# Performance work log

Measured on AMD Instinct MI355X. Metric: run time of the kernel, lower is better.

## Reference

```python
import jax, jax.numpy as jnp
import numpy as np

N = 100000
E = 1_600_000
DIN = 24
DH = 64
DOUT = 12
NEG_SLOPE = 0.01  # torch F.leaky_relu default


def setup_inputs() -> dict:
    key = jax.random.key(0)
    ks = jax.random.split(key, 18)
    inp = {}
    inp["feats"] = jax.random.normal(ks[0], (N, DIN), dtype=jnp.float32)
    inp["e_w"] = jax.random.uniform(ks[1], (E, 1), dtype=jnp.float32)
    inp["snorm_n"] = jnp.ones((N, 1), dtype=jnp.float32)
    inp["snorm_e"] = jnp.ones((E, 1), dtype=jnp.float32)
    inp["src"] = jax.random.randint(ks[2], (E,), 0, N, dtype=jnp.int32)
    inp["dst"] = jax.random.randint(ks[3], (E,), 0, N, dtype=jnp.int32)
    s = 0.05
    inp["emb_h_W"] = jax.random.normal(ks[4], (DH, DIN), dtype=jnp.float32) * s
    inp["emb_h_b"] = jnp.zeros((DH,), dtype=jnp.float32)
    inp["emb_e_W"] = jax.random.normal(ks[5], (DH, 1), dtype=jnp.float32) * s
    inp["emb_e_b"] = jnp.zeros((DH,), dtype=jnp.float32)
    inp["W_self1"] = jax.random.normal(ks[6], (DH, DH), dtype=jnp.float32) * s
    inp["W_func1"] = jax.random.normal(ks[7], (DH, DH), dtype=jnp.float32) * s
    inp["attn1"] = jax.random.normal(ks[8], (3 * DH,), dtype=jnp.float32) * s
    inp["W_self2"] = jax.random.normal(ks[9], (DH, DH), dtype=jnp.float32) * s
    inp["W_func2"] = jax.random.normal(ks[10], (DH, DH), dtype=jnp.float32) * s
    inp["attn2"] = jax.random.normal(ks[11], (3 * DH,), dtype=jnp.float32) * s
    inp["lin1_W"] = jax.random.normal(ks[12], (DOUT, DH), dtype=jnp.float32) * s
    inp["lin1_b"] = jnp.zeros((DOUT,), dtype=jnp.float32)
    return inp


def _gat_layer(h, w_edge, src, dst, W_self, W_func, attn):
    # h: [N, d], w_edge: [E, d] edge embedding, attn: [3d]
    h_s = h @ W_self.T                       # linear_self(h)
    z = h @ W_func.T                         # linear_func(h)
    d = z.shape[-1]
    a_src, a_dst, a_w = attn[:d], attn[d:2 * d], attn[2 * d:]
    # attention score: W_a . [z_src, z_dst, w]  (decomposed to avoid [E,3d] concat)
    s_node_src = z @ a_src                   # [N]
    s_node_dst = z @ a_dst                   # [N]
    e = s_node_src[src] + s_node_dst[dst] + w_edge @ a_w  # [E]
    e = jax.nn.leaky_relu(e, NEG_SLOPE)
    # segment softmax over incoming edges per destination node
    m = jax.ops.segment_max(e, dst, num_segments=h.shape[0])
    ex = jnp.exp(e - m[dst])
    denom = jax.ops.segment_sum(ex, dst, num_segments=h.shape[0])
    alpha = ex / denom[dst]                  # [E]
    msg = alpha[:, None] * z[src]            # [E, d]
    agg = jax.ops.segment_sum(msg, dst, num_segments=h.shape[0])  # [N, d]
    # DGL: nodes with no incoming edges keep their old 'h' (not h_s + agg)
    in_deg = jax.ops.segment_sum(jnp.ones_like(e), dst, num_segments=h.shape[0])
    h_mid = jnp.where((in_deg > 0)[:, None], h_s + agg, h)
    return h + jax.nn.relu(h_mid)            # relu then residual


def reference(feats, e_w, snorm_n, snorm_e, src, dst,
              emb_h_W, emb_h_b, emb_e_W, emb_e_b,
              W_self1, W_func1, attn1, W_self2, W_func2, attn2,
              lin1_W, lin1_b):
    feats = feats.reshape(feats.shape[0], -1)
    h = feats @ emb_h_W.T + emb_h_b          # [N, DH]
    e = e_w @ emb_e_W.T + emb_e_b            # [E, DH]
    h = _gat_layer(h, e, src, dst, W_self1, W_func1, attn1)
    h = _gat_layer(h, e, src, dst, W_self2, W_func2, attn2)
    y = h @ lin1_W.T + lin1_b                # [N, DOUT]
    return y
```

## Files before the change

kernel.cpp:

```cpp
#include <hip/hip_runtime.h>
#include <hip/hip_fp16.h>

#define N_NODES 100000
#define N_EDGES 1600000
#define DIN 24
#define DH 64
#define DOUT 12
#define NEG_SLOPE 0.01f
#define NG 64
#define EPG (N_EDGES / NG)
#define NS 4
#define SLICE_N 32768
#define NTOT (NG * N_NODES)
#define SCAN_BLK 4096
#define LDSW 72

#define NB_HIST (NS * NG)
#define NB_SUMDEG ((N_NODES + 255) / 256)
#define NB_SCAN1N ((N_NODES + SCAN_BLK - 1) / SCAN_BLK)
#define NB_SCAT ((N_EDGES / 4 + 255) / 256)
#define NB_NODE ((N_NODES + 63) / 64)
#define NB_NODE_T ((NB_NODE + 1) / 2)
#define NB_NME ((NB_NODE + 7) / 8)
#define NB_AGG ((N_NODES + 7) / 8)

#define SM_WEMB 18432
#define SM_BIAS 23552
#define SM_HBUF 23808
#define SM_SIZE 60672

typedef _Float16 half8_t __attribute__((ext_vector_type(8)));
typedef float floatx4 __attribute__((ext_vector_type(4)));

__device__ __forceinline__ void dev_consts(const float* emb_e_W, const float* emb_e_b,
                                           const float* attn1, const float* attn2,
                                           float* consts) {
    int lane = threadIdx.x;
    if (lane >= 64) return;
    float w = emb_e_W[lane], b = emb_e_b[lane];
    float a1 = attn1[2 * DH + lane], a2 = attn2[2 * DH + lane];
    float c11 = w * a1, c01 = b * a1, c12 = w * a2, c02 = b * a2;
    for (int off = 32; off; off >>= 1) {
        c11 += __shfl_down(c11, off);
        c01 += __shfl_down(c01, off);
        c12 += __shfl_down(c12, off);
        c02 += __shfl_down(c02, off);
    }
    if (lane == 0) {
        consts[0] = c11; consts[1] = c01; consts[2] = c12; consts[3] = c02;
    }
}

__device__ __forceinline__ void dev_hist(int bid, char* smem, const int* dst,
                                         unsigned char* deg, unsigned char* rank) {
    unsigned* cnt = (unsigned*)smem;
    int s = bid % NS, c = bid / NS;
    for (int i = threadIdx.x; i < SLICE_N / 4; i += 1024) cnt[i] = 0;
    __syncthreads();
    int nbase = s * SLICE_N;
    int start = c * EPG, end = start + EPG;
    for (int i = start + threadIdx.x; i < end; i += 1024) {
        int local = dst[i] - nbase;
        if ((unsigned)local < SLICE_N) {
            unsigned sh = (unsigned)(local & 3) * 8u;
            unsigned old = atomicAdd(&cnt[local >> 2], 1u << sh);
            rank[i] = (unsigned char)((old >> sh) & 255u);
        }
    }
    __syncthreads();
    int nmax = N_NODES - nbase;
    if (nmax > SLICE_N) nmax = SLICE_N;
    unsigned* dw = (unsigned*)(deg + (size_t)c * N_NODES + nbase);
    for (int l = threadIdx.x; l < (nmax >> 2); l += 1024) dw[l] = cnt[l];
}

__device__ __forceinline__ void dev_scan1(int bid, const int* in, int* out,
                                          int* part, int n) {
    __shared__ int lds[256];
    int t = threadIdx.x;
    int base = bid * SCAN_BLK + t * 16;
    int v[16];
    int s = 0;
#pragma unroll
    for (int i = 0; i < 16; ++i) {
        int idx = base + i;
        v[i] = (idx < n) ? in[idx] : 0;
        s += v[i];
    }
    lds[t] = s;
    __syncthreads();
    for (int off = 1; off < 256; off <<= 1) {
        int y = (t >= off) ? lds[t - off] : 0;
        __syncthreads();
        lds[t] += y;
        __syncthreads();
    }
    int run = lds[t] - s;
#pragma unroll
    for (int i = 0; i < 16; ++i) {
        int idx = base + i;
        if (idx < n) out[idx] = run;
        run += v[i];
    }
    if (t == 255) part[bid] = lds[255];
}

__device__ __forceinline__ void dev_sumdeg(int bid, const unsigned char* degB,
                                           int* degN, unsigned char* chunkOff) {
    int n = bid * 256 + threadIdx.x;
    if (n >= N_NODES) return;
    int run = 0;
    for (int g = 0; g < NG; ++g) {
        size_t idx = (size_t)g * N_NODES + n;
        int v = (int)degB[idx];
        chunkOff[idx] = (unsigned char)run;
        run += v;
    }
    degN[n] = run;
}

__device__ __forceinline__ void dev_nodeME(int bid, char* smem,
                                           const float* feats, const float* embW,
                                           const float* embB,
                                           const float* Wself, const float* Wfunc,
                                           const float* attn,
                                           __half* h16, __half* zh, __half* hs16,
                                           float* s_src, float* s_dst) {
    _Float16* lds   = (_Float16*)smem;
    _Float16* wembH = (_Float16*)(smem + SM_WEMB);
    float*    biasS = (float*)(smem + SM_BIAS);
    _Float16* hbufA = (_Float16*)(smem + SM_HBUF);
    int tid = threadIdx.x;
    for (int idx = tid; idx < 2 * 64 * 64; idx += 1024) {
        int mat = idx >> 12, rem = idx & 4095;
        int o = rem >> 6, k = rem & 63;
        float v = mat ? Wfunc[rem] : Wself[rem];
        lds[(mat * 64 + o) * LDSW + k] = (_Float16)v;
    }
    for (int idx = tid; idx < 64 * 32; idx += 1024) {
        int o = idx >> 5, k = idx & 31;
        wembH[o * 40 + k] = (_Float16)((k < DIN) ? embW[o * DIN + k] : 0.f);
    }
    if (tid < 64) biasS[tid] = embB[tid];
    __syncthreads();

    int wave = tid >> 6, lane = tid & 63;
    int vb = wave >> 2, wv = wave & 3;
    int quad = lane >> 4, lm = lane & 15;
    float asv[4], adv[4];
#pragma unroll
    for (int t = 0; t < 4; ++t) {
        asv[t] = attn[t * 16 + lm];
        adv[t] = attn[DH + t * 16 + lm];
    }
    const _Float16* bS = lds;
    const _Float16* bF = lds + 64 * LDSW;
    _Float16* hb = hbufA + wave * (16 * 72);

    for (int tb = bid * 4 + vb; tb < NB_NODE; tb += NB_NME * 4) {
        int n0 = (tb * 4 + wv) * 16;
        if (n0 >= N_NODES) continue;

        half8_t afE;
#pragma unroll
        for (int j = 0; j < 8; ++j) afE[j] = (_Float16)0.f;
        if (quad < 3) {
            const float* f = feats + (size_t)(n0 + lm) * DIN + quad * 8;
            float4 q0 = *(const float4*)(f);
            float4 q1 = *(const float4*)(f + 4);
            afE[0] = (_Float16)q0.x; afE[1] = (_Float16)q0.y;
            afE[2] = (_Float16)q0.z; afE[3] = (_Float16)q0.w;
            afE[4] = (_Float16)q1.x; afE[5] = (_Float16)q1.y;
            afE[6] = (_Float16)q1.z; afE[7] = (_Float16)q1.w;
        }
        floatx4 accE[4];
#pragma unroll
        for (int t = 0; t < 4; ++t) accE[t] = (floatx4)0.f;
#pragma unroll
        for (int t = 0; t < 4; ++t) {
            int o = t * 16 + lm;
            half8_t bE = *(const half8_t*)(wembH + o * 40 + quad * 8);
            accE[t] = __builtin_amdgcn_mfma_f32_16x16x32_f16(afE, bE, accE[t], 0, 0, 0);
        }
#pragma unroll
        for (int t = 0; t < 4; ++t) {
            float bv = biasS[t * 16 + lm];
#pragma unroll
            for (int r = 0; r < 4; ++r) {
                float hv = accE[t][r] + bv;
                int node = n0 + quad * 4 + r;
                h16[(size_t)node * DH + t * 16 + lm] = __float2half(hv);
                hb[(quad * 4 + r) * 72 + t * 16 + lm] = (_Float16)hv;
            }
        }
        half8_t afrag[2];
#pragma unroll
        for (int ks = 0; ks < 2; ++ks)
            afrag[ks] = *(const half8_t*)(hb + lm * 72 + ks * 32 + quad * 8);

        floatx4 accS[4], accF[4];
#pragma unroll
        for (int t = 0; t < 4; ++t) { accS[t] = (floatx4)0.f; accF[t] = (floatx4)0.f; }
#pragma unroll
        for (int t = 0; t < 4; ++t) {
            int o = t * 16 + lm;
#pragma unroll
            for (int ks = 0; ks < 2; ++ks) {
                int hoff = o * LDSW + ks * 32 + quad * 8;
                half8_t b1 = *(const half8_t*)(bS + hoff);
                half8_t b2 = *(const half8_t*)(bF + hoff);
                accS[t] = __builtin_amdgcn_mfma_f32_16x16x32_f16(afrag[ks], b1, accS[t], 0, 0, 0);
                accF[t] = __builtin_amdgcn_mfma_f32_16x16x32_f16(afrag[ks], b2, accF[t], 0, 0, 0);
            }
        }

        float ps[4] = {0.f, 0.f, 0.f, 0.f}, pd[4] = {0.f, 0.f, 0.f, 0.f};
#pragma unroll
        for (int t = 0; t < 4; ++t) {
#pragma unroll
            for (int r = 0; r < 4; ++r) {
                int node = n0 + quad * 4 + r;
                float zv = accF[t][r];
                zh[(size_t)node * DH + t * 16 + lm] = __float2half(zv);
                hs16[(size_t)node * DH + t * 16 + lm] = __float2half(accS[t][r]);
                ps[r] += zv * asv[t];
                pd[r] += zv * adv[t];
            }
        }
#pragma unroll
        for (int r = 0; r < 4; ++r) {
            float p1 = ps[r], p2 = pd[r];
            for (int off = 8; off; off >>= 1) {
                p1 += __shfl_xor(p1, off);
                p2 += __shfl_xor(p2, off);
            }
            if (lm == 0) {
                s_src[n0 + quad * 4 + r] = p1;
                s_dst[n0 + quad * 4 + r] = p2;
            }
        }
    }
}

__device__ __forceinline__ void dev_nodeM(int bid, int stride, const __half* h16,
                                          const float* Wself, const float* Wfunc,
                                          const float* attn,
                                          __half* zh, __half* hs16,
                                          float* s_src, float* s_dst) {
    __shared__ _Float16 lds[2 * 64 * LDSW];
    int tid = threadIdx.x;
    for (int idx = tid; idx < 2 * 64 * 64; idx += 256) {
        int mat = idx >> 12, rem = idx & 4095;
        int o = rem >> 6, k = rem & 63;
        float v = mat ? Wfunc[rem] : Wself[rem];
        lds[(mat * 64 + o) * LDSW + k] = (_Float16)v;
    }
    __syncthreads();

    int wave = tid >> 6, lane = tid & 63;
    int quad = lane >> 4, lm = lane & 15;
    float asv[4], adv[4];
#pragma unroll
    for (int t = 0; t < 4; ++t) {
        asv[t] = attn[t * 16 + lm];
        adv[t] = attn[DH + t * 16 + lm];
    }
    const _Float16* bS = lds;
    const _Float16* bF = lds + 64 * LDSW;

    for (int tb = bid; tb < NB_NODE; tb += stride) {
        int n0 = (tb * 4 + wave) * 16;
        if (n0 >= N_NODES) continue;

        const _Float16* hrow = (const _Float16*)h16 + (size_t)(n0 + lm) * DH;
        half8_t afrag[2];
#pragma unroll
        for (int ks = 0; ks < 2; ++ks)
            afrag[ks] = *(const half8_t*)(hrow + ks * 32 + quad * 8);

        floatx4 accS[4], accF[4];
#pragma unroll
        for (int t = 0; t < 4; ++t) { accS[t] = (floatx4)0.f; accF[t] = (floatx4)0.f; }

#pragma unroll
        for (int t = 0; t < 4; ++t) {
            int o = t * 16 + lm;
#pragma unroll
            for (int ks = 0; ks < 2; ++ks) {
                int hoff = o * LDSW + ks * 32 + quad * 8;
                half8_t b1 = *(const half8_t*)(bS + hoff);
                half8_t b2 = *(const half8_t*)(bF + hoff);
                accS[t] = __builtin_amdgcn_mfma_f32_16x16x32_f16(afrag[ks], b1, accS[t], 0, 0, 0);
                accF[t] = __builtin_amdgcn_mfma_f32_16x16x32_f16(afrag[ks], b2, accF[t], 0, 0, 0);
            }
        }

        float ps[4] = {0.f, 0.f, 0.f, 0.f}, pd[4] = {0.f, 0.f, 0.f, 0.f};
#pragma unroll
        for (int t = 0; t < 4; ++t) {
#pragma unroll
            for (int r = 0; r < 4; ++r) {
                int node = n0 + quad * 4 + r;
                float zv = accF[t][r];
                zh[(size_t)node * DH + t * 16 + lm] = __float2half(zv);
                hs16[(size_t)node * DH + t * 16 + lm] = __float2half(accS[t][r]);
                ps[r] += zv * asv[t];
                pd[r] += zv * adv[t];
            }
        }
#pragma unroll
        for (int r = 0; r < 4; ++r) {
            float p1 = ps[r], p2 = pd[r];
            for (int off = 8; off; off >>= 1) {
                p1 += __shfl_xor(p1, off);
                p2 += __shfl_xor(p2, off);
            }
            if (lm == 0) {
                s_src[n0 + quad * 4 + r] = p1;
                s_dst[n0 + quad * 4 + r] = p2;
            }
        }
    }
}

__global__ void __launch_bounds__(1024, 2)
k_fuse1(const int* __restrict__ dst, unsigned char* __restrict__ deg,
        unsigned char* __restrict__ rank,
        const float* __restrict__ emb_e_W, const float* __restrict__ emb_e_b,
        const float* __restrict__ attn1, const float* __restrict__ attn2,
        float* __restrict__ consts,
        const float* __restrict__ feats, const float* __restrict__ embW,
        const float* __restrict__ embB,
        __half* __restrict__ h16, const float* __restrict__ Wself1,
        const float* __restrict__ Wfunc1,
        __half* __restrict__ zh, __half* __restrict__ hs16,
        float* __restrict__ s_src, float* __restrict__ s_dst) {
    __shared__ __align__(16) char smem[SM_SIZE];
    int bid = blockIdx.x;
    if (bid == 0) { dev_consts(emb_e_W, emb_e_b, attn1, attn2, consts); return; }
    bid -= 1;
    if (bid < NB_HIST) { dev_hist(bid, smem, dst, deg, rank); return; }
    dev_nodeME(bid - NB_HIST, smem, feats, embW, embB, Wself1, Wfunc1, attn1,
               h16, zh, hs16, s_src, s_dst);
}

__global__ void k_prep2(const unsigned char* __restrict__ degB, int* __restrict__ degN,
                        unsigned char* __restrict__ chunkOff) {
    dev_sumdeg(blockIdx.x, degB, degN, chunkOff);
}

__global__ void k_prep3(const int* __restrict__ degN, int* __restrict__ row_offN,
                        int* __restrict__ partN) {
    dev_scan1(blockIdx.x, degN, row_offN, partN, N_NODES);
}

__global__ void k_prep4(const int* __restrict__ row_offN, const int* __restrict__ partN,
                        int* __restrict__ rowStart) {
    __shared__ int pfx[32];
    int t = threadIdx.x;
    if (t < 64) {
        int v = (t < NB_SCAN1N) ? partN[t] : 0;
        int x = v;
#pragma unroll
        for (int s = 1; s < 32; s <<= 1) {
            int y = __shfl_up(x, s);
            if (t >= s) x += y;
        }
        if (t < 32) pfx[t] = x - v;
    }
    __syncthreads();
    int n = blockIdx.x * 256 + t;
    if (n < N_NODES) rowStart[n] = row_offN[n] + pfx[n >> 12];
    if (n == 0) rowStart[N_NODES] = N_EDGES;
}

__global__ void __launch_bounds__(256, 8)
k_scat(const int* __restrict__ src, const int* __restrict__ dst,
       const float* __restrict__ e_w, const unsigned char* __restrict__ rank,
       const int* __restrict__ rowStart,
       const unsigned char* __restrict__ chunkOff, unsigned* __restrict__ csr2) {
    int e4 = (blockIdx.x * 256 + threadIdx.x) * 4;
    if (e4 >= N_EDGES) return;
    int g = e4 / EPG;
    const unsigned char* co = chunkOff + (size_t)g * N_NODES;
    int4   d4 = *(const int4*)(dst + e4);
    int4   s4 = *(const int4*)(src + e4);
    float4 w4 = *(const float4*)(e_w + e4);
    unsigned r4 = *(const unsigned*)(rank + e4);
    int b0 = rowStart[d4.x] + (int)co[d4.x];
    int b1 = rowStart[d4.y] + (int)co[d4.y];
    int b2 = rowStart[d4.z] + (int)co[d4.z];
    int b3 = rowStart[d4.w] + (int)co[d4.w];
    unsigned q0 = (unsigned)(w4.x * 32768.f); if (q0 > 32767u) q0 = 32767u;
    unsigned q1 = (unsigned)(w4.y * 32768.f); if (q1 > 32767u) q1 = 32767u;
    unsigned q2 = (unsigned)(w4.z * 32768.f); if (q2 > 32767u) q2 = 32767u;
    unsigned q3 = (unsigned)(w4.w * 32768.f); if (q3 > 32767u) q3 = 32767u;
    __builtin_nontemporal_store((unsigned)s4.x | (q0 << 17), csr2 + b0 + (r4 & 255u));
    __builtin_nontemporal_store((unsigned)s4.y | (q1 << 17), csr2 + b1 + ((r4 >> 8) & 255u));
    __builtin_nontemporal_store((unsigned)s4.z | (q2 << 17), csr2 + b2 + ((r4 >> 16) & 255u));
    __builtin_nontemporal_store((unsigned)s4.w | (q3 << 17), csr2 + b3 + (r4 >> 24));
}

__global__ void __launch_bounds__(256, 4)
k_nodeL(const __half* __restrict__ h16, const float* __restrict__ Wself,
        const float* __restrict__ Wfunc, const float* __restrict__ attn,
        __half* __restrict__ zh, __half* __restrict__ hs16,
        float* __restrict__ s_src, float* __restrict__ s_dst) {
    dev_nodeM(blockIdx.x, NB_NODE_T, h16, Wself, Wfunc, attn, zh, hs16, s_src, s_dst);
}

__global__ void k_agg(const int* __restrict__ rowStart,
                      const unsigned* __restrict__ csr,
                      const float* __restrict__ s_src, const float* __restrict__ s_dstA,
                      const float* __restrict__ consts, int layer,
                      const __half* __restrict__ zh, const __half* __restrict__ hsb,
                      __half* __restrict__ h16,
                      const float* __restrict__ lin_W, const float* __restrict__ lin_b,
                      float* __restrict__ y, int final_layer) {
    int wave = threadIdx.x >> 6, lane = threadIdx.x & 63;
    int half = lane >> 5, hl = lane & 31;
    int eg = (lane >> 3) & 3, c8 = lane & 7;
    int n = blockIdx.x * 8 + wave * 2 + half;
    if (n >= N_NODES) return;
    int rs = rowStart[n];
    int deg = rowStart[n + 1] - rs;
    int degO = __shfl_xor(deg, 32);
    int degmax = deg > degO ? deg : degO;

    float c1 = consts[layer * 2 + 0];
    float c0 = consts[layer * 2 + 1];
    float sd = s_dstA[n];

    float acc[8];
#pragma unroll
    for (int k = 0; k < 8; ++k) acc[k] = 0.f;
    float ssl = 0.f;
    int lbase = lane & 32;

    for (int base = 0; base < degmax; base += 32) {
        float ex = 0.f;
        int s0 = 0;
        int idx = base + hl;
        if (idx < deg) {
            unsigned w = csr[rs + idx];
            s0 = (int)(w & 0x1FFFFu);
            float ew = (float)(w >> 17) * (1.f / 32768.f);
            float e = s_src[s0] + sd + ew * c1 + c0;
            e = (e > 0.f) ? e : NEG_SLOPE * e;
            ex = __expf(e);
        }
        ssl += ex;
        int cnt = degmax - base;
        if (cnt > 32) cnt = 32;
#pragma unroll 4
        for (int jb = 0; jb < cnt; jb += 4) {
            int srcl = lbase + jb + eg;
            int sj = __shfl(s0, srcl);
            float exj = __shfl(ex, srcl);
            unsigned boff = ((unsigned)sj << 7) | ((unsigned)c8 << 4);
            half8_t zv = *(const half8_t*)((const char*)zh + boff);
#pragma unroll
            for (int k = 0; k < 8; ++k) acc[k] += exj * (float)zv[k];
        }
    }
#pragma unroll
    for (int k = 0; k < 8; ++k) {
        acc[k] += __shfl_xor(acc[k], 8);
        acc[k] += __shfl_xor(acc[k], 16);
    }
    ssl += __shfl_xor(ssl, 16); ssl += __shfl_xor(ssl, 8);
    ssl += __shfl_xor(ssl, 4);  ssl += __shfl_xor(ssl, 2);
    ssl += __shfl_xor(ssl, 1);

    unsigned noff = ((unsigned)n << 7) | ((unsigned)c8 << 4);
    half8_t hv8 = *(const half8_t*)((const char*)h16 + noff);
    float hold[8];
#pragma unroll
    for (int k = 0; k < 8; ++k) hold[k] = (float)hv8[k];
    float hnew[8];
    if (deg == 0) {
#pragma unroll
        for (int k = 0; k < 8; ++k) hnew[k] = hold[k] + fmaxf(hold[k], 0.f);
    } else {
        float rinv = 1.f / ssl;
        half8_t hs8 = *(const half8_t*)((const char*)hsb + noff);
#pragma unroll
        for (int k = 0; k < 8; ++k)
            hnew[k] = hold[k] + fmaxf((float)hs8[k] + acc[k] * rinv, 0.f);
    }

    if (!final_layer) {
        if (eg == 0) {
            half8_t o8;
#pragma unroll
            for (int k = 0; k < 8; ++k) o8[k] = (_Float16)hnew[k];
            *(half8_t*)((char*)h16 + noff) = o8;
        }
    } else {
#pragma unroll
        for (int t = 0; t < 3; ++t) {
            int o = eg * 3 + t;
            const float* wr = lin_W + o * DH + c8 * 8;
            float p = 0.f;
#pragma unroll
            for (int k = 0; k < 8; ++k) p += hnew[k] * wr[k];
            p += __shfl_xor(p, 1); p += __shfl_xor(p, 2); p += __shfl_xor(p, 4);
            if (c8 == 0) y[n * DOUT + o] = p + lin_b[o];
        }
    }
}

extern "C" void kernel_launch(void* const* d_in, const int* in_sizes, int n_in,
                              void* d_out, int out_size, void* d_ws, size_t ws_size,
                              hipStream_t stream) {
    const float* feats   = (const float*)d_in[0];
    const float* e_w     = (const float*)d_in[1];
    const int*   src     = (const int*)d_in[4];
    const int*   dst     = (const int*)d_in[5];
    const float* emb_h_W = (const float*)d_in[6];
    const float* emb_h_b = (const float*)d_in[7];
    const float* emb_e_W = (const float*)d_in[8];
    const float* emb_e_b = (const float*)d_in[9];
    const float* Wself[2] = {(const float*)d_in[10], (const float*)d_in[13]};
    const float* Wfunc[2] = {(const float*)d_in[11], (const float*)d_in[14]};
    const float* attn[2]  = {(const float*)d_in[12], (const float*)d_in[15]};
    const float* lin1_W  = (const float*)d_in[16];
    const float* lin1_b  = (const float*)d_in[17];
    float* y = (float*)d_out;

    char* ws = (char*)d_ws;
    size_t off = 0;
    auto alloc = [&](size_t bytes) {
        void* p = ws + off;
        off += (bytes + 255) & ~(size_t)255;
        return p;
    };
    __half*         h16      = (__half*)alloc((size_t)N_NODES * DH * 2);
    __half*         zh       = (__half*)alloc((size_t)N_NODES * DH * 2);
    __half*         hs16     = (__half*)alloc((size_t)N_NODES * DH * 2);
    unsigned*       csr2     = (unsigned*)alloc((size_t)N_EDGES * 4);
    float*          s_src    = (float*)alloc((size_t)N_NODES * 4);
    float*          s_dst    = (float*)alloc((size_t)N_NODES * 4);
    int*            row_offN = (int*)alloc((size_t)(N_NODES + 1) * 4);
    int*            rowStart = (int*)alloc((size_t)(N_NODES + 1) * 4);
    unsigned char*  deg      = (unsigned char*)alloc((size_t)NTOT + 256);
    unsigned char*  chunkOff = (unsigned char*)alloc((size_t)NTOT + 256);
    unsigned char*  rank     = (unsigned char*)alloc((size_t)N_EDGES);
    int*            degN     = (int*)alloc((size_t)N_NODES * 4);
    int*            partN    = (int*)alloc(1024 * 4);
    float*          consts   = (float*)alloc(4 * 4);

    k_fuse1<<<1 + NB_HIST + NB_NME, 1024, 0, stream>>>(
        dst, deg, rank, emb_e_W, emb_e_b, attn[0], attn[1], consts,
        feats, emb_h_W, emb_h_b, h16, Wself[0], Wfunc[0], zh, hs16, s_src, s_dst);
    k_prep2<<<NB_SUMDEG, 256, 0, stream>>>(deg, degN, chunkOff);
    k_prep3<<<NB_SCAN1N, 256, 0, stream>>>(degN, row_offN, partN);
    k_prep4<<<NB_SUMDEG, 256, 0, stream>>>(row_offN, partN, rowStart);
    k_scat<<<NB_SCAT, 256, 0, stream>>>(src, dst, e_w, rank, rowStart,
                                        chunkOff, csr2);
    k_agg<<<NB_AGG, 256, 0, stream>>>(rowStart, csr2, s_src, s_dst, consts, 0,
                                      zh, hs16, h16, lin1_W, lin1_b, y, 0);
    k_nodeL<<<NB_NODE_T, 256, 0, stream>>>(h16, Wself[1], Wfunc[1], attn[1],
                                           zh, hs16, s_src, s_dst);
    k_agg<<<NB_AGG, 256, 0, stream>>>(rowStart, csr2, s_src, s_dst, consts, 1,
                                      zh, hs16, h16, lin1_W, lin1_b, y, 1);
}
```

Before: 295.8 us.

## Move node embedding/linear work from histogram kernel into scatter kernel launch

The layer-1 node embedding and linear transform blocks are taken out of the histogram kernel and co-launched with the CSR scatter in a new fused kernel with 1024-thread blocks. The histogram kernel now uses a smaller shared-memory allocation, which may allow more blocks per CU. The scatter drops its nontemporal stores and now runs as 1024-thread blocks that share a launch with the shared-memory-heavy node blocks. This rebalances which independent work overlaps, at the cost of possibly worse scatter occupancy and write caching behaviour.

```diff
diff --git a/kernel.cpp b/kernel.cpp
--- a/kernel.cpp
+++ b/kernel.cpp
@@ -18,7 +18,7 @@
 #define NB_HIST (NS * NG)
 #define NB_SUMDEG ((N_NODES + 255) / 256)
 #define NB_SCAN1N ((N_NODES + SCAN_BLK - 1) / SCAN_BLK)
-#define NB_SCAT ((N_EDGES / 4 + 255) / 256)
+#define NB_SCAT4 ((N_EDGES / 4 + 1023) / 1024)
 #define NB_NODE ((N_NODES + 63) / 64)
 #define NB_NODE_T ((NB_NODE + 1) / 2)
 #define NB_NME ((NB_NODE + 7) / 8)
@@ -117,6 +117,33 @@
         run += v;
     }
     degN[n] = run;
+}
+
+__device__ __forceinline__ void dev_scat4(int bid, const int* src, const int* dst,
+                                          const float* e_w, const unsigned char* rank,
+                                          const int* rowStart,
+                                          const unsigned char* chunkOff,
+                                          unsigned* csr2) {
+    int e4 = (bid * 1024 + threadIdx.x) * 4;
+    if (e4 >= N_EDGES) return;
+    int g = e4 / EPG;
+    const unsigned char* co = chunkOff + (size_t)g * N_NODES;
+    int4   d4 = *(const int4*)(dst + e4);
+    int4   s4 = *(const int4*)(src + e4);
+    float4 w4 = *(const float4*)(e_w + e4);
+    unsigned r4 = *(const unsigned*)(rank + e4);
+    int b0 = rowStart[d4.x] + (int)co[d4.x];
+    int b1 = rowStart[d4.y] + (int)co[d4.y];
+    int b2 = rowStart[d4.z] + (int)co[d4.z];
+    int b3 = rowStart[d4.w] + (int)co[d4.w];
+    unsigned q0 = (unsigned)(w4.x * 32768.f); if (q0 > 32767u) q0 = 32767u;
+    unsigned q1 = (unsigned)(w4.y * 32768.f); if (q1 > 32767u) q1 = 32767u;
+    unsigned q2 = (unsigned)(w4.z * 32768.f); if (q2 > 32767u) q2 = 32767u;
+    unsigned q3 = (unsigned)(w4.w * 32768.f); if (q3 > 32767u) q3 = 32767u;
+    csr2[b0 + (r4 & 255u)]         = (unsigned)s4.x | (q0 << 17);
+    csr2[b1 + ((r4 >> 8) & 255u)]  = (unsigned)s4.y | (q1 << 17);
+    csr2[b2 + ((r4 >> 16) & 255u)] = (unsigned)s4.z | (q2 << 17);
+    csr2[b3 + (r4 >> 24)]          = (unsigned)s4.w | (q3 << 17);
 }
 
 __device__ __forceinline__ void dev_nodeME(int bid, char* smem,
@@ -328,20 +355,11 @@
         unsigned char* __restrict__ rank,
         const float* __restrict__ emb_e_W, const float* __restrict__ emb_e_b,
         const float* __restrict__ attn1, const float* __restrict__ attn2,
-        float* __restrict__ consts,
-        const float* __restrict__ feats, const float* __restrict__ embW,
-        const float* __restrict__ embB,
-        __half* __restrict__ h16, const float* __restrict__ Wself1,
-        const float* __restrict__ Wfunc1,
-        __half* __restrict__ zh, __half* __restrict__ hs16,
-        float* __restrict__ s_src, float* __restrict__ s_dst) {
-    __shared__ __align__(16) char smem[SM_SIZE];
+        float* __restrict__ consts) {
+    __shared__ __align__(16) char smem[SLICE_N];
     int bid = blockIdx.x;
     if (bid == 0) { dev_consts(emb_e_W, emb_e_b, attn1, attn2, consts); return; }
-    bid -= 1;
-    if (bid < NB_HIST) { dev_hist(bid, smem, dst, deg, rank); return; }
-    dev_nodeME(bid - NB_HIST, smem, feats, embW, embB, Wself1, Wfunc1, attn1,
-               h16, zh, hs16, s_src, s_dst);
+    dev_hist(bid - 1, smem, dst, deg, rank);
 }
 
 __global__ void k_prep2(const unsigned char* __restrict__ degB, int* __restrict__ degN,
@@ -374,31 +392,25 @@
     if (n == 0) rowStart[N_NODES] = N_EDGES;
 }
 
-__global__ void __launch_bounds__(256, 8)
-k_scat(const int* __restrict__ src, const int* __restrict__ dst,
-       const float* __restrict__ e_w, const unsigned char* __restrict__ rank,
-       const int* __restrict__ rowStart,
-       const unsigned char* __restrict__ chunkOff, unsigned* __restrict__ csr2) {
-    int e4 = (blockIdx.x * 256 + threadIdx.x) * 4;
-    if (e4 >= N_EDGES) return;
-    int g = e4 / EPG;
-    const unsigned char* co = chunkOff + (size_t)g * N_NODES;
-    int4   d4 = *(const int4*)(dst + e4);
-    int4   s4 = *(const int4*)(src + e4);
-    float4 w4 = *(const float4*)(e_w + e4);
-    unsigned r4 = *(const unsigned*)(rank + e4);
-    int b0 = rowStart[d4.x] + (int)co[d4.x];
-    int b1 = rowStart[d4.y] + (int)co[d4.y];
-    int b2 = rowStart[d4.z] + (int)co[d4.z];
-    int b3 = rowStart[d4.w] + (int)co[d4.w];
-    unsigned q0 = (unsigned)(w4.x * 32768.f); if (q0 > 32767u) q0 = 32767u;
-    unsigned q1 = (unsigned)(w4.y * 32768.f); if (q1 > 32767u) q1 = 32767u;
-    unsigned q2 = (unsigned)(w4.z * 32768.f); if (q2 > 32767u) q2 = 32767u;
-    unsigned q3 = (unsigned)(w4.w * 32768.f); if (q3 > 32767u) q3 = 32767u;
-    __builtin_nontemporal_store((unsigned)s4.x | (q0 << 17), csr2 + b0 + (r4 & 255u));
-    __builtin_nontemporal_store((unsigned)s4.y | (q1 << 17), csr2 + b1 + ((r4 >> 8) & 255u));
-    __builtin_nontemporal_store((unsigned)s4.z | (q2 << 17), csr2 + b2 + ((r4 >> 16) & 255u));
-    __builtin_nontemporal_store((unsigned)s4.w | (q3 << 17), csr2 + b3 + (r4 >> 24));
+__global__ void __launch_bounds__(1024, 2)
+k_fuse5(const float* __restrict__ feats, const float* __restrict__ embW,
+        const float* __restrict__ embB,
+        __half* __restrict__ h16, const float* __restrict__ Wself1,
+        const float* __restrict__ Wfunc1, const float* __restrict__ attn1,
+        __half* __restrict__ zh, __half* __restrict__ hs16,
+        float* __restrict__ s_src, float* __restrict__ s_dst,
+        const int* __restrict__ src, const int* __restrict__ dst,
+        const float* __restrict__ e_w, const unsigned char* __restrict__ rank,
+        const int* __restrict__ rowStart,
+        const unsigned char* __restrict__ chunkOff, unsigned* __restrict__ csr2) {
+    __shared__ __align__(16) char smem[SM_SIZE];
+    int bid = blockIdx.x;
+    if (bid < NB_NME) {
+        dev_nodeME(bid, smem, feats, embW, embB, Wself1, Wfunc1, attn1,
+                   h16, zh, hs16, s_src, s_dst);
+        return;
+    }
+    dev_scat4(bid - NB_NME, src, dst, e_w, rank, rowStart, chunkOff, csr2);
 }
 
 __global__ void __launch_bounds__(256, 4)
@@ -550,14 +562,15 @@
     int*            partN    = (int*)alloc(1024 * 4);
     float*          consts   = (float*)alloc(4 * 4);
 
-    k_fuse1<<<1 + NB_HIST + NB_NME, 1024, 0, stream>>>(
-        dst, deg, rank, emb_e_W, emb_e_b, attn[0], attn[1], consts,
-        feats, emb_h_W, emb_h_b, h16, Wself[0], Wfunc[0], zh, hs16, s_src, s_dst);
+    k_fuse1<<<1 + NB_HIST, 1024, 0, stream>>>(dst, deg, rank, emb_e_W, emb_e_b,
+                                              attn[0], attn[1], consts);
     k_prep2<<<NB_SUMDEG, 256, 0, stream>>>(deg, degN, chunkOff);
     k_prep3<<<NB_SCAN1N, 256, 0, stream>>>(degN, row_offN, partN);
     k_prep4<<<NB_SUMDEG, 256, 0, stream>>>(row_offN, partN, rowStart);
-    k_scat<<<NB_SCAT, 256, 0, stream>>>(src, dst, e_w, rank, rowStart,
-                                        chunkOff, csr2);
+    k_fuse5<<<NB_NME + NB_SCAT4, 1024, 0, stream>>>(
+        feats, emb_h_W, emb_h_b, h16, Wself[0], Wfunc[0], attn[0],
+        zh, hs16, s_src, s_dst,
+        src, dst, e_w, rank, rowStart, chunkOff, csr2);
     k_agg<<<NB_AGG, 256, 0, stream>>>(rowStart, csr2, s_src, s_dst, consts, 0,
                                       zh, hs16, h16, lin1_W, lin1_b, y, 0);
     k_nodeL<<<NB_NODE_T, 256, 0, stream>>>(h16, Wself[1], Wfunc[1], attn[1],
```

Result: faster. 286.7 us (-3.1%).
